# Kernel tuning notes

Measured on AMD Instinct MI355X. Metric: run time of the kernel, lower is better.

The kernel has to match this reference:

```python
import jax, jax.numpy as jnp
import numpy as np

B, T, H, L = 64, 1024, 1024, 2


def setup_inputs() -> dict:
    key = jax.random.key(0)
    ks = jax.random.split(key, 5)
    stdv = 1.0 / np.sqrt(H)
    u = lambda k, shape: jax.random.uniform(k, shape, jnp.float32, -stdv, stdv)
    return {
        "Xt": jax.random.normal(ks[0], (B, T, H), jnp.float32),
        "Wih": u(ks[1], (L, H, H)),
        "bih": u(ks[2], (L, H)),
        "Whh": u(ks[3], (L, H, H)),
        "bhh": u(ks[4], (L, H)),
    }


def reference(Xt, Wih, bih, Whh, bhh):
    # Stacked Elman RNN, batch_first, zero initial hidden state, tanh, dropout=0.
    # h: [L, B, H] stacked per-layer hidden states.
    h0 = jnp.zeros((L, B, H), Xt.dtype)

    def step(h, x_t):  # h: [L,B,H], x_t: [B,H]
        x = x_t
        new_h = []
        for i in range(L):
            x = jnp.tanh(x @ Wih[i].T + bih[i] + h[i] @ Whh[i].T + bhh[i])
            new_h.append(x)
        return jnp.stack(new_h), x  # carry new hidden, emit top-layer output

    xs = jnp.swapaxes(Xt, 0, 1)  # [T, B, H]
    hT, ys = jax.lax.scan(step, h0, xs)
    out = jnp.swapaxes(ys, 0, 1)  # [B, T, H]
    return (out, hT)
```

## Files before the change

kernel.cpp:

```cpp
#include <hip/hip_runtime.h>
#include <hip/hip_bf16.h>
#include <stdint.h>

#define HH 1024
#define BB 64
#define TT 1024

typedef __attribute__((ext_vector_type(8))) short short8;
typedef __attribute__((ext_vector_type(4))) float f32x4;

__device__ __forceinline__ unsigned short f2bf(float f) {
  union { float f; unsigned u; } v; v.f = f;
  unsigned r = v.u + 0x7fffu + ((v.u >> 16) & 1u);
  return (unsigned short)(r >> 16);
}

__global__ void prep_kernel(const float* __restrict__ Wih, const float* __restrict__ Whh,
                            const float* __restrict__ bih, const float* __restrict__ bhh,
                            unsigned short* __restrict__ wih_b, unsigned short* __restrict__ whh_b,
                            float* __restrict__ bias01) {
  int i = blockIdx.x * 256 + threadIdx.x;
  wih_b[i] = f2bf(Wih[i]);
  whh_b[i] = f2bf(Whh[i]);
  if (i < 2 * HH) bias01[i] = bih[i] + bhh[i];
}

__device__ __forceinline__ size_t rowperm(int r) {
  return ((size_t)(r & 63) << 10) | (size_t)(r >> 6);
}

template<bool ABF16, bool APERM, bool CPERM>
__global__ __launch_bounds__(256)
void gemm_bias(const void* __restrict__ Av, const unsigned short* __restrict__ Wb,
               const float* __restrict__ bias, float* __restrict__ Gout) {
  __shared__ unsigned short As[128 * 40];
  __shared__ unsigned short Bs[128 * 40];
  const int tn = blockIdx.x & 7;
  const int tm = blockIdx.x >> 3;
  const int tid = threadIdx.x;
  const int wid = tid >> 6, lane = tid & 63;
  const int wr = (wid >> 1) * 64, wc = (wid & 1) * 64;
  const int l15 = lane & 15, l4 = lane >> 4;
  f32x4 acc[4][4] = {};

  const float* Af = (const float*)Av;
  const unsigned short* Ab = (const unsigned short*)Av;
  const int sr = tid >> 2;
  const int sk = (tid & 3) * 8;

  for (int k0 = 0; k0 < HH; k0 += 32) {
    __syncthreads();
#pragma unroll
    for (int p = 0; p < 2; ++p) {
      const int row = p * 64 + sr;
      const int rg = tm * 128 + row;
      const size_t ar = APERM ? rowperm(rg) : (size_t)rg;
      if (ABF16) {
        const unsigned short* src = Ab + ar * HH + k0 + sk;
        *(short8*)&As[row * 40 + sk] = *(const short8*)src;
      } else {
        const float* src = Af + ar * HH + k0 + sk;
        float4 x = *(const float4*)src;
        float4 y = *(const float4*)(src + 4);
        short8 v;
        v[0] = (short)f2bf(x.x); v[1] = (short)f2bf(x.y);
        v[2] = (short)f2bf(x.z); v[3] = (short)f2bf(x.w);
        v[4] = (short)f2bf(y.x); v[5] = (short)f2bf(y.y);
        v[6] = (short)f2bf(y.z); v[7] = (short)f2bf(y.w);
        *(short8*)&As[row * 40 + sk] = v;
      }
      const unsigned short* wsrc = Wb + (size_t)(tn * 128 + row) * HH + k0 + sk;
      *(short8*)&Bs[row * 40 + sk] = *(const short8*)wsrc;
    }
    __syncthreads();
    short8 a[4], b[4];
#pragma unroll
    for (int i = 0; i < 4; ++i) a[i] = *(short8*)&As[(wr + i * 16 + l15) * 40 + l4 * 8];
#pragma unroll
    for (int j = 0; j < 4; ++j) b[j] = *(short8*)&Bs[(wc + j * 16 + l15) * 40 + l4 * 8];
#pragma unroll
    for (int i = 0; i < 4; ++i)
#pragma unroll
      for (int j = 0; j < 4; ++j)
        acc[i][j] = __builtin_amdgcn_mfma_f32_16x16x32_bf16(a[i], b[j], acc[i][j], 0, 0, 0);
  }
#pragma unroll
  for (int j = 0; j < 4; ++j) {
    const int gc = tn * 128 + wc + j * 16 + l15;
    const float bv = bias[gc];
#pragma unroll
    for (int i = 0; i < 4; ++i) {
#pragma unroll
      for (int jj = 0; jj < 4; ++jj) {
        const int gr = tm * 128 + wr + i * 16 + l4 * 4 + jj;
        const size_t orow = CPERM ? rowperm(gr) : (size_t)gr;
        Gout[orow * HH + gc] = acc[i][j][jj] + bv;
      }
    }
  }
}

template<int LAYER>
__global__ __launch_bounds__(256)
void rec_layer(const float* G,
               const unsigned short* __restrict__ Whh_b,
               unsigned short* __restrict__ ping,
               unsigned short* __restrict__ h0s,
               float* outf,
               float* __restrict__ hT,
               unsigned int* flags) {
  const int g = blockIdx.x;
  const int tid = threadIdx.x, wid = tid >> 6, lane = tid & 63;
  const int l15 = lane & 15, l4 = lane >> 4, kp = l4 * 8;
  __shared__ unsigned short Wl[16 * 1032];

  for (int idx = tid; idx < 16 * 64; idx += 256) {
    const int j = idx >> 6, kseg = (idx & 63) * 16;
    const short8* src = (const short8*)&Whh_b[(size_t)(g * 16 + j) * HH + kseg];
    *(short8*)&Wl[j * 1032 + kseg] = src[0];
    *(short8*)&Wl[j * 1032 + kseg + 8] = src[1];
  }
  __syncthreads();

  const int col = g * 16 + l15;
  const unsigned short* brow = (const unsigned short*)&Wl[l15 * 1032 + kp];
  const uint64_t myflag = (uint64_t)(flags + (size_t)g * 256);
  const uint64_t pollflag = (uint64_t)(flags + (size_t)lane * 256);

  int bidx[4];
#pragma unroll
  for (int jj = 0; jj < 4; ++jj) bidx[jj] = wid * 16 + l4 * 4 + jj;

  float gv[4], gn[4];
#pragma unroll
  for (int jj = 0; jj < 4; ++jj) {
    const size_t gi = (LAYER == 0) ? ((size_t)(0 * BB + bidx[jj])) * HH + col
                                   : ((size_t)(bidx[jj] * TT + 0)) * HH + col;
    gv[jj] = G[gi];
  }

  for (int t = 0; t < TT; ++t) {
    if (t + 1 < TT) {
#pragma unroll
      for (int jj = 0; jj < 4; ++jj) {
        const size_t gi = (LAYER == 0) ? ((size_t)((t + 1) * BB + bidx[jj])) * HH + col
                                       : ((size_t)(bidx[jj] * TT + (t + 1))) * HH + col;
        gn[jj] = G[gi];
      }
    }

    f32x4 acc0 = {}, acc1 = {};
    if (t > 0) {
      const unsigned short* hprev = ping + ((t - 1) & 1) * (BB * HH);
      const unsigned short* arow = hprev + (size_t)(wid * 16 + l15) * HH + kp;
#pragma unroll
      for (int ks = 0; ks < 32; ks += 2) {
        short8 a0 = *(const short8*)(arow + ks * 32);
        short8 b0 = *(const short8*)(brow + ks * 32);
        acc0 = __builtin_amdgcn_mfma_f32_16x16x32_bf16(a0, b0, acc0, 0, 0, 0);
        short8 a1 = *(const short8*)(arow + (ks + 1) * 32);
        short8 b1 = *(const short8*)(brow + (ks + 1) * 32);
        acc1 = __builtin_amdgcn_mfma_f32_16x16x32_bf16(a1, b1, acc1, 0, 0, 0);
      }
    }

    unsigned short* hcur = ping + (t & 1) * (BB * HH);
#pragma unroll
    for (int jj = 0; jj < 4; ++jj) {
      const int b = bidx[jj];
      const size_t gidx = (LAYER == 0) ? ((size_t)(t * BB + b)) * HH + col
                                       : ((size_t)(b * TT + t)) * HH + col;
      const float pre = acc0[jj] + acc1[jj] + gv[jj];
      const float h = tanhf(pre);
      const unsigned short hb = f2bf(h);
      {
        const uint64_t ha = (uint64_t)(hcur + (size_t)b * HH + col);
        asm volatile("global_store_short %0, %1, off sc0 sc1"
                     :: "v"(ha), "v"((unsigned)hb) : "memory");
      }
      if (LAYER == 0) h0s[gidx] = hb;
      else            outf[gidx] = h;
      if (t == TT - 1) hT[b * HH + col] = h;
    }

    asm volatile("s_waitcnt vmcnt(0)" ::: "memory");
    __syncthreads();
    if (tid == 0) {
      const unsigned val = (unsigned)(t + 1);
      asm volatile("s_waitcnt vmcnt(0)\n\t"
                   "global_store_dword %0, %1, off sc0 sc1"
                   :: "v"(myflag), "v"(val) : "memory");
    }
    if (wid == 0) {
      const unsigned tgt = (unsigned)(t + 1);
      unsigned v;
      do {
        asm volatile("global_load_dword %0, %1, off sc0 sc1\n\t"
                     "s_waitcnt vmcnt(0)"
                     : "=v"(v) : "v"(pollflag) : "memory");
      } while (!__all((int)(v >= tgt)));
      __builtin_amdgcn_fence(__ATOMIC_ACQUIRE, "agent");
    }
    __syncthreads();

#pragma unroll
    for (int jj = 0; jj < 4; ++jj) gv[jj] = gn[jj];
  }
}

extern "C" void kernel_launch(void* const* d_in, const int* in_sizes, int n_in,
                              void* d_out, int out_size, void* d_ws, size_t ws_size,
                              hipStream_t stream) {
  const float* Xt  = (const float*)d_in[0];
  const float* Wih = (const float*)d_in[1];
  const float* bih = (const float*)d_in[2];
  const float* Whh = (const float*)d_in[3];
  const float* bhh = (const float*)d_in[4];
  float* out = (float*)d_out;
  float* hT  = out + (size_t)BB * TT * HH;

  char* ws = (char*)d_ws;
  unsigned short* wih_b  = (unsigned short*)(ws);
  unsigned short* whh_b  = (unsigned short*)(ws + (4u << 20));
  float*          bias01 = (float*)(ws + (8u << 20));
  unsigned short* h0buf  = (unsigned short*)(ws + (16u << 20));
  unsigned short* ping   = (unsigned short*)(ws + (160u << 20));
  unsigned int*   flags  = (unsigned int*)(ws + (161u << 20));

  if (ws_size < (162u << 20)) return;

  hipMemsetAsync(flags, 0, 128 * 1024, stream);
  prep_kernel<<<8192, 256, 0, stream>>>(Wih, Whh, bih, bhh, wih_b, whh_b, bias01);

  gemm_bias<false, true, false><<<4096, 256, 0, stream>>>(Xt, wih_b, bias01, out);

  {
    const float* G = out;
    const unsigned short* W = whh_b;
    unsigned short* pg = ping;
    unsigned short* h0s = h0buf;
    float* of = nullptr;
    float* ht = hT;
    unsigned int* fl = flags;
    void* args[] = {&G, &W, &pg, &h0s, &of, &ht, &fl};
    hipLaunchCooperativeKernel((void*)rec_layer<0>, dim3(64), dim3(256), args, 0, stream);
  }

  gemm_bias<true, false, true><<<4096, 256, 0, stream>>>(h0buf, wih_b + (size_t)HH * HH,
                                                         bias01 + HH, out);

  {
    const float* G = out;
    const unsigned short* W = whh_b + (size_t)HH * HH;
    unsigned short* pg = ping + 2 * (size_t)BB * HH;
    unsigned short* h0s = h0buf;
    float* of = out;
    float* ht = hT + (size_t)BB * HH;
    unsigned int* fl = flags + (64u * 1024u / 4u);
    void* args[] = {&G, &W, &pg, &h0s, &of, &ht, &fl};
    hipLaunchCooperativeKernel((void*)rec_layer<1>, dim3(64), dim3(256), args, 0, stream);
  }
}
```

Baseline: 14.37 ms.

## Fuse both RNN layers into one wavefront-pipelined persistent cooperative kernel

Replaces the two sequential recurrent kernels and the intermediate layer-1 input GEMM with a single cooperative kernel. Layer 1 at step t-1 runs alongside layer 0 at step t, so one grid barrier per step serves both layers and the 1024 serial steps are no longer paid twice. Layer 1's input projection is now computed inside the recurrence with an extra 1024-K MFMA pass per step, using Wih1 and Whh1 held in LDS. The layer-0 precomputed input is stored as fp16 to halve its traffic, tanh uses an exp/rcp approximation, and the flags are packed contiguously. This adds per-step compute, more LDS per block, and some precision loss from fp16 storage and the approximate tanh.

```diff
diff --git a/kernel.cpp b/kernel.cpp
--- a/kernel.cpp
+++ b/kernel.cpp
@@ -13,6 +13,17 @@
   union { float f; unsigned u; } v; v.f = f;
   unsigned r = v.u + 0x7fffu + ((v.u >> 16) & 1u);
   return (unsigned short)(r >> 16);
+}
+
+__device__ __forceinline__ float h2f(unsigned short u) {
+  _Float16 h;
+  __builtin_memcpy(&h, &u, 2);
+  return (float)h;
+}
+
+__device__ __forceinline__ float ftanh(float x) {
+  float e = __expf(2.0f * x);
+  return 1.0f - 2.0f * __builtin_amdgcn_rcpf(e + 1.0f);
 }
 
 __global__ void prep_kernel(const float* __restrict__ Wih, const float* __restrict__ Whh,
@@ -29,10 +40,10 @@
   return ((size_t)(r & 63) << 10) | (size_t)(r >> 6);
 }
 
-template<bool ABF16, bool APERM, bool CPERM>
+template<bool ABF16, bool APERM, bool CPERM, bool OUTF16>
 __global__ __launch_bounds__(256)
 void gemm_bias(const void* __restrict__ Av, const unsigned short* __restrict__ Wb,
-               const float* __restrict__ bias, float* __restrict__ Gout) {
+               const float* __restrict__ bias, void* __restrict__ GoutV) {
   __shared__ unsigned short As[128 * 40];
   __shared__ unsigned short Bs[128 * 40];
   const int tn = blockIdx.x & 7;
@@ -94,38 +105,51 @@
       for (int jj = 0; jj < 4; ++jj) {
         const int gr = tm * 128 + wr + i * 16 + l4 * 4 + jj;
         const size_t orow = CPERM ? rowperm(gr) : (size_t)gr;
-        Gout[orow * HH + gc] = acc[i][j][jj] + bv;
-      }
-    }
-  }
-}
-
-template<int LAYER>
+        const float val = acc[i][j][jj] + bv;
+        if (OUTF16) ((_Float16*)GoutV)[orow * HH + gc] = (_Float16)val;
+        else        ((float*)GoutV)[orow * HH + gc] = val;
+      }
+    }
+  }
+}
+
 __global__ __launch_bounds__(256)
-void rec_layer(const float* G,
-               const unsigned short* __restrict__ Whh_b,
-               unsigned short* __restrict__ ping,
-               unsigned short* __restrict__ h0s,
-               float* outf,
+void rec_fused(const unsigned short* __restrict__ Gh,
+               const unsigned short* __restrict__ Whh0_b,
+               const unsigned short* __restrict__ Wih1_b,
+               const unsigned short* __restrict__ Whh1_b,
+               const float* __restrict__ bias1,
+               unsigned short* __restrict__ h0p,
+               unsigned short* __restrict__ h1p,
+               float* __restrict__ outp,
                float* __restrict__ hT,
                unsigned int* flags) {
   const int g = blockIdx.x;
   const int tid = threadIdx.x, wid = tid >> 6, lane = tid & 63;
   const int l15 = lane & 15, l4 = lane >> 4, kp = l4 * 8;
-  __shared__ unsigned short Wl[16 * 1032];
+  __shared__ unsigned short Wl0[16 * 1032];
+  __shared__ unsigned short Wl1[16 * 2056];
 
   for (int idx = tid; idx < 16 * 64; idx += 256) {
     const int j = idx >> 6, kseg = (idx & 63) * 16;
-    const short8* src = (const short8*)&Whh_b[(size_t)(g * 16 + j) * HH + kseg];
-    *(short8*)&Wl[j * 1032 + kseg] = src[0];
-    *(short8*)&Wl[j * 1032 + kseg + 8] = src[1];
+    const short8* s0 = (const short8*)&Whh0_b[(size_t)(g * 16 + j) * HH + kseg];
+    *(short8*)&Wl0[j * 1032 + kseg] = s0[0];
+    *(short8*)&Wl0[j * 1032 + kseg + 8] = s0[1];
+    const short8* s1 = (const short8*)&Wih1_b[(size_t)(g * 16 + j) * HH + kseg];
+    *(short8*)&Wl1[j * 2056 + kseg] = s1[0];
+    *(short8*)&Wl1[j * 2056 + kseg + 8] = s1[1];
+    const short8* s2 = (const short8*)&Whh1_b[(size_t)(g * 16 + j) * HH + kseg];
+    *(short8*)&Wl1[j * 2056 + 1024 + kseg] = s2[0];
+    *(short8*)&Wl1[j * 2056 + 1024 + kseg + 8] = s2[1];
   }
   __syncthreads();
 
   const int col = g * 16 + l15;
-  const unsigned short* brow = (const unsigned short*)&Wl[l15 * 1032 + kp];
-  const uint64_t myflag = (uint64_t)(flags + (size_t)g * 256);
-  const uint64_t pollflag = (uint64_t)(flags + (size_t)lane * 256);
+  const unsigned short* b0row = &Wl0[l15 * 1032 + kp];
+  const unsigned short* b1row = &Wl1[l15 * 2056 + kp];
+  const float bc1 = bias1[col];
+  const uint64_t myflag = (uint64_t)(flags + g);
+  const uint64_t pollflag = (uint64_t)(flags + lane);
 
   int bidx[4];
 #pragma unroll
@@ -133,78 +157,112 @@
 
   float gv[4], gn[4];
 #pragma unroll
-  for (int jj = 0; jj < 4; ++jj) {
-    const size_t gi = (LAYER == 0) ? ((size_t)(0 * BB + bidx[jj])) * HH + col
-                                   : ((size_t)(bidx[jj] * TT + 0)) * HH + col;
-    gv[jj] = G[gi];
-  }
-
-  for (int t = 0; t < TT; ++t) {
-    if (t + 1 < TT) {
+  for (int jj = 0; jj < 4; ++jj) gv[jj] = h2f(Gh[(size_t)bidx[jj] * HH + col]);
+
+  for (int p = 0; p <= TT; ++p) {
+    if (p + 1 < TT) {
+#pragma unroll
+      for (int jj = 0; jj < 4; ++jj)
+        gn[jj] = h2f(Gh[((size_t)(p + 1) * BB + bidx[jj]) * HH + col]);
+    }
+
+    if (p < TT) {
+      f32x4 acc0 = {}, acc1 = {};
+      if (p > 0) {
+        const unsigned short* arow =
+            h0p + ((p - 1) & 1) * (BB * HH) + (size_t)(wid * 16 + l15) * HH + kp;
+#pragma unroll
+        for (int ks = 0; ks < 32; ks += 2) {
+          short8 a0 = *(const short8*)(arow + ks * 32);
+          short8 w0 = *(const short8*)(b0row + ks * 32);
+          acc0 = __builtin_amdgcn_mfma_f32_16x16x32_bf16(a0, w0, acc0, 0, 0, 0);
+          short8 a1 = *(const short8*)(arow + (ks + 1) * 32);
+          short8 w1 = *(const short8*)(b0row + (ks + 1) * 32);
+          acc1 = __builtin_amdgcn_mfma_f32_16x16x32_bf16(a1, w1, acc1, 0, 0, 0);
+        }
+      }
+      unsigned short* hc = h0p + (p & 1) * (BB * HH);
 #pragma unroll
       for (int jj = 0; jj < 4; ++jj) {
-        const size_t gi = (LAYER == 0) ? ((size_t)((t + 1) * BB + bidx[jj])) * HH + col
-                                       : ((size_t)(bidx[jj] * TT + (t + 1))) * HH + col;
-        gn[jj] = G[gi];
-      }
-    }
-
-    f32x4 acc0 = {}, acc1 = {};
-    if (t > 0) {
-      const unsigned short* hprev = ping + ((t - 1) & 1) * (BB * HH);
-      const unsigned short* arow = hprev + (size_t)(wid * 16 + l15) * HH + kp;
-#pragma unroll
-      for (int ks = 0; ks < 32; ks += 2) {
-        short8 a0 = *(const short8*)(arow + ks * 32);
-        short8 b0 = *(const short8*)(brow + ks * 32);
-        acc0 = __builtin_amdgcn_mfma_f32_16x16x32_bf16(a0, b0, acc0, 0, 0, 0);
-        short8 a1 = *(const short8*)(arow + (ks + 1) * 32);
-        short8 b1 = *(const short8*)(brow + (ks + 1) * 32);
-        acc1 = __builtin_amdgcn_mfma_f32_16x16x32_bf16(a1, b1, acc1, 0, 0, 0);
-      }
-    }
-
-    unsigned short* hcur = ping + (t & 1) * (BB * HH);
-#pragma unroll
-    for (int jj = 0; jj < 4; ++jj) {
-      const int b = bidx[jj];
-      const size_t gidx = (LAYER == 0) ? ((size_t)(t * BB + b)) * HH + col
-                                       : ((size_t)(b * TT + t)) * HH + col;
-      const float pre = acc0[jj] + acc1[jj] + gv[jj];
-      const float h = tanhf(pre);
-      const unsigned short hb = f2bf(h);
-      {
-        const uint64_t ha = (uint64_t)(hcur + (size_t)b * HH + col);
+        const float pre = acc0[jj] + acc1[jj] + gv[jj];
+        const float h = ftanh(pre);
+        const unsigned short hb = f2bf(h);
+        const uint64_t ha = (uint64_t)(hc + (size_t)bidx[jj] * HH + col);
         asm volatile("global_store_short %0, %1, off sc0 sc1"
                      :: "v"(ha), "v"((unsigned)hb) : "memory");
-      }
-      if (LAYER == 0) h0s[gidx] = hb;
-      else            outf[gidx] = h;
-      if (t == TT - 1) hT[b * HH + col] = h;
-    }
-
-    asm volatile("s_waitcnt vmcnt(0)" ::: "memory");
-    __syncthreads();
-    if (tid == 0) {
-      const unsigned val = (unsigned)(t + 1);
-      asm volatile("s_waitcnt vmcnt(0)\n\t"
-                   "global_store_dword %0, %1, off sc0 sc1"
-                   :: "v"(myflag), "v"(val) : "memory");
-    }
-    if (wid == 0) {
-      const unsigned tgt = (unsigned)(t + 1);
-      unsigned v;
-      do {
-        asm volatile("global_load_dword %0, %1, off sc0 sc1\n\t"
-                     "s_waitcnt vmcnt(0)"
-                     : "=v"(v) : "v"(pollflag) : "memory");
-      } while (!__all((int)(v >= tgt)));
-      __builtin_amdgcn_fence(__ATOMIC_ACQUIRE, "agent");
-    }
-    __syncthreads();
-
-#pragma unroll
-    for (int jj = 0; jj < 4; ++jj) gv[jj] = gn[jj];
+        if (p == TT - 1) hT[(size_t)bidx[jj] * HH + col] = h;
+      }
+    }
+
+    if (p >= 1) {
+      const int t1 = p - 1;
+      f32x4 acc0 = {}, acc1 = {};
+      {
+        const unsigned short* arow =
+            h0p + (t1 & 1) * (BB * HH) + (size_t)(wid * 16 + l15) * HH + kp;
+#pragma unroll
+        for (int ks = 0; ks < 32; ks += 2) {
+          short8 a0 = *(const short8*)(arow + ks * 32);
+          short8 w0 = *(const short8*)(b1row + ks * 32);
+          acc0 = __builtin_amdgcn_mfma_f32_16x16x32_bf16(a0, w0, acc0, 0, 0, 0);
+          short8 a1 = *(const short8*)(arow + (ks + 1) * 32);
+          short8 w1 = *(const short8*)(b1row + (ks + 1) * 32);
+          acc1 = __builtin_amdgcn_mfma_f32_16x16x32_bf16(a1, w1, acc1, 0, 0, 0);
+        }
+      }
+      if (t1 > 0) {
+        const unsigned short* arow =
+            h1p + ((t1 - 1) & 1) * (BB * HH) + (size_t)(wid * 16 + l15) * HH + kp;
+#pragma unroll
+        for (int ks = 0; ks < 32; ks += 2) {
+          short8 a0 = *(const short8*)(arow + ks * 32);
+          short8 w0 = *(const short8*)(b1row + 1024 + ks * 32);
+          acc0 = __builtin_amdgcn_mfma_f32_16x16x32_bf16(a0, w0, acc0, 0, 0, 0);
+          short8 a1 = *(const short8*)(arow + (ks + 1) * 32);
+          short8 w1 = *(const short8*)(b1row + 1024 + (ks + 1) * 32);
+          acc1 = __builtin_amdgcn_mfma_f32_16x16x32_bf16(a1, w1, acc1, 0, 0, 0);
+        }
+      }
+      unsigned short* hc = h1p + (t1 & 1) * (BB * HH);
+#pragma unroll
+      for (int jj = 0; jj < 4; ++jj) {
+        const float pre = acc0[jj] + acc1[jj] + bc1;
+        const float h = ftanh(pre);
+        outp[((size_t)bidx[jj] * TT + t1) * HH + col] = h;
+        if (t1 < TT - 1) {
+          const unsigned short hb = f2bf(h);
+          const uint64_t ha = (uint64_t)(hc + (size_t)bidx[jj] * HH + col);
+          asm volatile("global_store_short %0, %1, off sc0 sc1"
+                       :: "v"(ha), "v"((unsigned)hb) : "memory");
+        } else {
+          hT[BB * HH + (size_t)bidx[jj] * HH + col] = h;
+        }
+      }
+    }
+
+    if (p < TT) {
+      asm volatile("s_waitcnt vmcnt(0)" ::: "memory");
+      __syncthreads();
+      if (tid == 0) {
+        const unsigned val = (unsigned)(p + 1);
+        asm volatile("s_waitcnt vmcnt(0)\n\t"
+                     "global_store_dword %0, %1, off sc0 sc1"
+                     :: "v"(myflag), "v"(val) : "memory");
+      }
+      if (wid == 0) {
+        const unsigned tgt = (unsigned)(p + 1);
+        unsigned v;
+        do {
+          asm volatile("global_load_dword %0, %1, off sc0 sc1\n\t"
+                       "s_waitcnt vmcnt(0)"
+                       : "=v"(v) : "v"(pollflag) : "memory");
+        } while (!__all((int)(v >= tgt)));
+        __builtin_amdgcn_fence(__ATOMIC_ACQUIRE, "agent");
+      }
+      __syncthreads();
+#pragma unroll
+      for (int jj = 0; jj < 4; ++jj) gv[jj] = gn[jj];
+    }
   }
 }
 
@@ -223,41 +281,30 @@
   unsigned short* wih_b  = (unsigned short*)(ws);
   unsigned short* whh_b  = (unsigned short*)(ws + (4u << 20));
   float*          bias01 = (float*)(ws + (8u << 20));
-  unsigned short* h0buf  = (unsigned short*)(ws + (16u << 20));
-  unsigned short* ping   = (unsigned short*)(ws + (160u << 20));
-  unsigned int*   flags  = (unsigned int*)(ws + (161u << 20));
-
-  if (ws_size < (162u << 20)) return;
-
-  hipMemsetAsync(flags, 0, 128 * 1024, stream);
+  unsigned short* Gh     = (unsigned short*)(ws + (16u << 20));
+  unsigned short* h0p    = (unsigned short*)(ws + (145u << 20));
+  unsigned short* h1p    = (unsigned short*)(ws + (146u << 20));
+  unsigned int*   flags  = (unsigned int*)(ws + (147u << 20));
+
+  if (ws_size < (150u << 20)) return;
+
+  hipMemsetAsync(flags, 0, 4096, stream);
   prep_kernel<<<8192, 256, 0, stream>>>(Wih, Whh, bih, bhh, wih_b, whh_b, bias01);
 
-  gemm_bias<false, true, false><<<4096, 256, 0, stream>>>(Xt, wih_b, bias01, out);
+  gemm_bias<false, true, false, true><<<4096, 256, 0, stream>>>(Xt, wih_b, bias01, Gh);
 
   {
-    const float* G = out;
-    const unsigned short* W = whh_b;
-    unsigned short* pg = ping;
-    unsigned short* h0s = h0buf;
-    float* of = nullptr;
+    const unsigned short* G = Gh;
+    const unsigned short* W0 = whh_b;
+    const unsigned short* W1i = wih_b + (size_t)HH * HH;
+    const unsigned short* W1h = whh_b + (size_t)HH * HH;
+    const float* b1 = bias01 + HH;
+    unsigned short* p0 = h0p;
+    unsigned short* p1 = h1p;
+    float* op = out;
     float* ht = hT;
     unsigned int* fl = flags;
-    void* args[] = {&G, &W, &pg, &h0s, &of, &ht, &fl};
-    hipLaunchCooperativeKernel((void*)rec_layer<0>, dim3(64), dim3(256), args, 0, stream);
-  }
-
-  gemm_bias<true, false, true><<<4096, 256, 0, stream>>>(h0buf, wih_b + (size_t)HH * HH,
-                                                         bias01 + HH, out);
-
-  {
-    const float* G = out;
-    const unsigned short* W = whh_b + (size_t)HH * HH;
-    unsigned short* pg = ping + 2 * (size_t)BB * HH;
-    unsigned short* h0s = h0buf;
-    float* of = out;
-    float* ht = hT + (size_t)BB * HH;
-    unsigned int* fl = flags + (64u * 1024u / 4u);
-    void* args[] = {&G, &W, &pg, &h0s, &of, &ht, &fl};
-    hipLaunchCooperativeKernel((void*)rec_layer<1>, dim3(64), dim3(256), args, 0, stream);
-  }
-}
+    void* args[] = {&G, &W0, &W1i, &W1h, &b1, &p0, &p1, &op, &ht, &fl};
+    hipLaunchCooperativeKernel((void*)rec_fused, dim3(64), dim3(256), args, 0, stream);
+  }
+}
```

Result: slower. 16.19 ms (+12.7%).
